# Performance work log

Hardware: AMD Instinct MI355X
Metric: run time of the kernel (lower is better)

Reference implementation:

```python
import jax, jax.numpy as jnp
import numpy as np


def _maxpool(x, k):
    # NCHW max pool with window k, stride k, no padding
    return jax.lax.reduce_window(
        x, -jnp.inf, jax.lax.max,
        window_dimensions=(1, 1, k, k),
        window_strides=(1, 1, k, k),
        padding='VALID')


def setup_inputs() -> dict:
    key = jax.random.key(0)
    k1, k2, k3, k4, k5 = jax.random.split(key, 5)
    return {
        'input_tensor1': jax.random.normal(k1, (8, 128, 56, 56), dtype=jnp.float32),
        'input_tensor2': jax.random.normal(k2, (8, 64, 112, 112), dtype=jnp.float32),
        'input_tensor3': jax.random.normal(k3, (8, 32, 224, 224), dtype=jnp.float32),
        'input_tensor4': jax.random.normal(k4, (8, 16, 448, 448), dtype=jnp.float32),
        'pure_ff': jax.random.normal(k5, (8, 256, 28, 28), dtype=jnp.float32),
    }


def reference(input_tensor1, input_tensor2, input_tensor3, input_tensor4, pure_ff):
    # Original: cat input k times along channels, then maxpool. Pooling is
    # channel-independent, so pool-once-then-tile is mathematically identical
    # (the cat pattern [x,x,...,x] is an exact channel tiling).
    x1 = jnp.tile(_maxpool(input_tensor1, 2), (1, 2, 1, 1))
    x2 = jnp.tile(_maxpool(input_tensor2, 4), (1, 4, 1, 1))
    x3 = jnp.tile(_maxpool(input_tensor3, 8), (1, 8, 1, 1))
    x4 = jnp.tile(_maxpool(input_tensor4, 16), (1, 16, 1, 1))
    return jax.nn.relu(x1 + x2 + x3 + x4 + pure_ff)
```

## Files before the change

kernel.cpp:

```cpp
#include <hip/hip_runtime.h>

#define DEVINL __device__ __forceinline__

DEVINL float fmax4(float4 v) { return fmaxf(fmaxf(v.x, v.y), fmaxf(v.z, v.w)); }
DEVINL float4 max44(float4 a, float4 b) {
    float4 r; r.x = fmaxf(a.x, b.x); r.y = fmaxf(a.y, b.y);
    r.z = fmaxf(a.z, b.z); r.w = fmaxf(a.w, b.w); return r;
}

#define MEMBAR() asm volatile("" ::: "memory")

#define P4O 0
#define P3O 448
#define P2O 1344
#define P1O 3136
#define SCRO 6720
#define LDS_FLOATS 13888

#define LD7(DST, PTR)                                                      \
    { _Pragma("unroll") for (int k = 0; k < 7; ++k)                        \
          DST[k] = *(const float4*)((PTR) + k * 256); }

#define LD7T2(DST, EOFF)                                                   \
    { _Pragma("unroll") for (int k = 0; k < 7; ++k) {                      \
          const int f = k * 64 + lane;                                     \
          DST[k] = *(const float4*)(base2 + (EOFF) + (f / 112) * 12544     \
                                    + (f % 112) * 4); } }

#define LD7T1(DST)                                                         \
    { _Pragma("unroll") for (int k = 0; k < 7; ++k) {                      \
          const int f = k * 64 + lane;                                     \
          DST[k] = *(const float4*)(base1 + (f / 28) * 3136                \
                                    + (f % 28) * 4); } }

#define ACCSET(V) { _Pragma("unroll") for (int k = 0; k < 7; ++k) acc[k] = V[k]; }
#define ACCMAX(V) { _Pragma("unroll") for (int k = 0; k < 7; ++k) acc[k] = max44(acc[k], V[k]); }

#define GATH4(E)                                                           \
    { _Pragma("unroll") for (int k = 0; k < 7; ++k)                        \
          sm[k * 64 + lane] = fmax4(acc[k]);                               \
      MEMBAR();                                                            \
      if (lane < 28) {                                                     \
          float4 ga = *(const float4*)&sm[0 * 112 + 4 * lane];             \
          float4 gb = *(const float4*)&sm[1 * 112 + 4 * lane];             \
          float4 gc = *(const float4*)&sm[2 * 112 + 4 * lane];             \
          float4 gd = *(const float4*)&sm[3 * 112 + 4 * lane];             \
          lds[P4O + (2 * ww + (E)) * 28 + lane] =                          \
              fmax4(max44(max44(ga, gb), max44(gc, gd))); } }

#define T3W(V, H)                                                          \
    { float* smh = sm + (H) * 448;                                         \
      _Pragma("unroll") for (int k = 0; k < 7; ++k)                        \
          smh[k * 64 + lane] = fmax4(V[k]); }
#define T3G(I, H)                                                          \
    { float* smh = sm + (H) * 448;                                         \
      if (lane < 28) {                                                     \
          float2 p0 = *(const float2*)&smh[2 * lane];                      \
          float m = fmaxf(p0.x, p0.y);                                     \
          _Pragma("unroll") for (int r = 1; r < 8; ++r) {                  \
              float2 pr = *(const float2*)&smh[r * 56 + 2 * lane];         \
              m = fmaxf(m, fmaxf(pr.x, pr.y)); }                          \
          lds[P3O + (4 * ww + (I)) * 28 + lane] = m; } }

#define T2W(V, H)                                                          \
    { float* smh = sm + (H) * 448;                                         \
      _Pragma("unroll") for (int k = 0; k < 7; ++k)                        \
          smh[k * 64 + lane] = fmax4(V[k]); }
#define T2G(E, H)                                                          \
    { float* smh = sm + (H) * 448;                                         \
      if (lane < 56) {                                                     \
          _Pragma("unroll") for (int h2 = 0; h2 < 2; ++h2) {               \
              const int o = lane + 56 * h2;                                \
              const int cc = o / 28, j = o % 28;                           \
              float m = fmaxf(fmaxf(smh[cc * 112 + 0 * 28 + j],            \
                                    smh[cc * 112 + 1 * 28 + j]),           \
                              fmaxf(smh[cc * 112 + 2 * 28 + j],            \
                                    smh[cc * 112 + 3 * 28 + j]));          \
              lds[P2O + (8 * ww + 4 * (E) + cc) * 28 + j] = m; } } }

#define T1W(V)                                                             \
    { _Pragma("unroll") for (int k = 0; k < 7; ++k) {                      \
          const int f = k * 64 + lane;                                     \
          float2 hh; hh.x = fmaxf(V[k].x, V[k].y);                         \
          hh.y = fmaxf(V[k].z, V[k].w);                                    \
          *(float2*)&sm[2 * f] = hh; } }
#define T1G()                                                              \
    { _Pragma("unroll") for (int h2 = 0; h2 < 7; ++h2) {                   \
          const int idx = h2 * 64 + lane;                                  \
          const int cc = idx / 28, j = idx % 28;                           \
          lds[P1O + (16 * ww + cc) * 28 + j] =                             \
              fmaxf(sm[cc * 56 + j], sm[cc * 56 + 28 + j]); } }

__global__ __launch_bounds__(512, 2) void fused_all(
    const float* __restrict__ t1, const float* __restrict__ t2,
    const float* __restrict__ t3, const float* __restrict__ t4,
    const float* __restrict__ ff, float* __restrict__ out)
{
    __shared__ __align__(16) float lds[LDS_FLOATS];
    const int tid  = threadIdx.x;
    const int lane = tid & 63;
    const int ww   = tid >> 6;
    const int ph   = blockIdx.x;
    const int b    = blockIdx.y;
    float* sm = &lds[SCRO + ww * 896];

    const float4* FF = (const float4*)ff;
    float4 ffr[4];
    #pragma unroll
    for (int m = 0; m < 3; ++m) {
        const int i4 = tid + 512 * m;
        ffr[m] = FF[(size_t)(b * 256 + i4 / 7) * 196 + ph * 7 + i4 % 7];
    }
    if (tid < 256) {
        const int i4 = tid + 1536;
        ffr[3] = FF[(size_t)(b * 256 + i4 / 7) * 196 + ph * 7 + i4 % 7];
    }

    const float* a4 = t4 + (size_t)b * 3211264 + (2 * ww) * 200704
                    + ph * 16 * 448 + 4 * lane;
    const float* b4 = a4 + 200704;
    const float* c3 = t3 + (size_t)b * 1605632 + (4 * ww) * 50176
                    + ph * 8 * 224 + 4 * lane;
    const float* base2 = t2 + (size_t)b * 802816 + (8 * ww) * 12544
                       + ph * 448;
    const float* base1 = t1 + (size_t)b * 401408 + (16 * ww) * 3136
                       + ph * 112;

    float4 A[7], B[7], acc[7];
    LD7(A, a4);
    LD7(B, a4 + 1792);
    MEMBAR();
    ACCSET(A);
    LD7(A, a4 + 3584); MEMBAR();
    ACCMAX(B);
    LD7(B, a4 + 5376); MEMBAR();
    ACCMAX(A);
    LD7(A, b4); MEMBAR();
    ACCMAX(B);
    LD7(B, b4 + 1792); MEMBAR();
    GATH4(0);
    ACCSET(A);
    LD7(A, b4 + 3584); MEMBAR();
    ACCMAX(B);
    LD7(B, b4 + 5376); MEMBAR();
    ACCMAX(A);
    LD7(A, c3); MEMBAR();
    ACCMAX(B);
    LD7(B, c3 + 50176); MEMBAR();
    GATH4(1);
    T3W(A, 0); LD7(A, c3 + 2 * 50176); MEMBAR(); T3G(0, 0);
    T3W(B, 1); LD7(B, c3 + 3 * 50176); MEMBAR(); T3G(1, 1);
    T3W(A, 0); LD7T2(A, 0);            MEMBAR(); T3G(2, 0);
    T3W(B, 1); LD7T2(B, 50176);        MEMBAR(); T3G(3, 1);
    T2W(A, 0); LD7T1(A);               MEMBAR(); T2G(0, 0);
    T2W(B, 1);                         MEMBAR(); T2G(1, 1);
    T1W(A); MEMBAR(); T1G();

    __syncthreads();

    float4* O = (float4*)out;
    #pragma unroll
    for (int m = 0; m < 4; ++m) {
        if (m < 3 || tid < 256) {
            const int i4 = tid + 512 * m;
            const int ch = i4 / 7, j4 = i4 % 7;
            const float4 x1 = *(const float4*)&lds[P1O + (ch & 127) * 28 + 4 * j4];
            const float4 x2 = *(const float4*)&lds[P2O + (ch & 63)  * 28 + 4 * j4];
            const float4 x3 = *(const float4*)&lds[P3O + (ch & 31)  * 28 + 4 * j4];
            const float4 x4 = *(const float4*)&lds[P4O + (ch & 15)  * 28 + 4 * j4];
            const float4 f  = ffr[m];
            float4 o;
            o.x = fmaxf(x1.x + x2.x + x3.x + x4.x + f.x, 0.0f);
            o.y = fmaxf(x1.y + x2.y + x3.y + x4.y + f.y, 0.0f);
            o.z = fmaxf(x1.z + x2.z + x3.z + x4.z + f.z, 0.0f);
            o.w = fmaxf(x1.w + x2.w + x3.w + x4.w + f.w, 0.0f);
            O[(size_t)(b * 256 + ch) * 196 + ph * 7 + j4] = o;
        }
    }
}

extern "C" void kernel_launch(void* const* d_in, const int* in_sizes, int n_in,
                              void* d_out, int out_size, void* d_ws, size_t ws_size,
                              hipStream_t stream) {
    const float* t1 = (const float*)d_in[0];
    const float* t2 = (const float*)d_in[1];
    const float* t3 = (const float*)d_in[2];
    const float* t4 = (const float*)d_in[3];
    const float* ff = (const float*)d_in[4];
    dim3 grid(28, 8);
    fused_all<<<grid, 512, 0, stream>>>(t1, t2, t3, t4, ff, (float*)d_out);
}
```

Before: 225.2 us.

## Use inline-asm global loads with explicit vmcnt waits and triple buffering

Replaces compiler-generated global loads with inline-asm global_load_dwordx4 and manual s_waitcnt vmcnt counters. A third register buffer lets up to three batches of loads stay in flight while the max reductions run. The ff prefetch is made unconditional with clamped indices so the vmcnt accounting stays fixed. This raises register pressure, and correctness now depends on the hand-counted waits, since the compiler no longer tracks these loads.

```diff
diff --git a/kernel.cpp b/kernel.cpp
--- a/kernel.cpp
+++ b/kernel.cpp
@@ -2,13 +2,22 @@
 
 #define DEVINL __device__ __forceinline__
 
-DEVINL float fmax4(float4 v) { return fmaxf(fmaxf(v.x, v.y), fmaxf(v.z, v.w)); }
-DEVINL float4 max44(float4 a, float4 b) {
-    float4 r; r.x = fmaxf(a.x, b.x); r.y = fmaxf(a.y, b.y);
+typedef float f4 __attribute__((ext_vector_type(4)));
+
+DEVINL float fmax4(f4 v) { return fmaxf(fmaxf(v.x, v.y), fmaxf(v.z, v.w)); }
+DEVINL f4 max44(f4 a, f4 b) {
+    f4 r; r.x = fmaxf(a.x, b.x); r.y = fmaxf(a.y, b.y);
     r.z = fmaxf(a.z, b.z); r.w = fmaxf(a.w, b.w); return r;
 }
 
-#define MEMBAR() asm volatile("" ::: "memory")
+DEVINL f4 ald(const float* p) {
+    f4 r;
+    asm volatile("global_load_dwordx4 %0, %1, off" : "=v"(r) : "v"(p));
+    return r;
+}
+#define VMW(N)                                                             \
+    asm volatile("s_waitcnt vmcnt(" #N ")" ::: "memory");                  \
+    __builtin_amdgcn_sched_barrier(0);
 
 #define P4O 0
 #define P3O 448
@@ -17,21 +26,19 @@
 #define SCRO 6720
 #define LDS_FLOATS 13888
 
-#define LD7(DST, PTR)                                                      \
+#define LD7G(DST, PTR)                                                     \
     { _Pragma("unroll") for (int k = 0; k < 7; ++k)                        \
-          DST[k] = *(const float4*)((PTR) + k * 256); }
+          DST[k] = ald((PTR) + k * 256); }
 
 #define LD7T2(DST, EOFF)                                                   \
     { _Pragma("unroll") for (int k = 0; k < 7; ++k) {                      \
           const int f = k * 64 + lane;                                     \
-          DST[k] = *(const float4*)(base2 + (EOFF) + (f / 112) * 12544     \
-                                    + (f % 112) * 4); } }
+          DST[k] = ald(base2 + (EOFF) + (f / 112) * 12544 + (f % 112) * 4); } }
 
 #define LD7T1(DST)                                                         \
     { _Pragma("unroll") for (int k = 0; k < 7; ++k) {                      \
           const int f = k * 64 + lane;                                     \
-          DST[k] = *(const float4*)(base1 + (f / 28) * 3136                \
-                                    + (f % 28) * 4); } }
+          DST[k] = ald(base1 + (f / 28) * 3136 + (f % 28) * 4); } }
 
 #define ACCSET(V) { _Pragma("unroll") for (int k = 0; k < 7; ++k) acc[k] = V[k]; }
 #define ACCMAX(V) { _Pragma("unroll") for (int k = 0; k < 7; ++k) acc[k] = max44(acc[k], V[k]); }
@@ -39,12 +46,11 @@
 #define GATH4(E)                                                           \
     { _Pragma("unroll") for (int k = 0; k < 7; ++k)                        \
           sm[k * 64 + lane] = fmax4(acc[k]);                               \
-      MEMBAR();                                                            \
       if (lane < 28) {                                                     \
-          float4 ga = *(const float4*)&sm[0 * 112 + 4 * lane];             \
-          float4 gb = *(const float4*)&sm[1 * 112 + 4 * lane];             \
-          float4 gc = *(const float4*)&sm[2 * 112 + 4 * lane];             \
-          float4 gd = *(const float4*)&sm[3 * 112 + 4 * lane];             \
+          f4 ga = *(const f4*)&sm[0 * 112 + 4 * lane];                     \
+          f4 gb = *(const f4*)&sm[1 * 112 + 4 * lane];                     \
+          f4 gc = *(const f4*)&sm[2 * 112 + 4 * lane];                     \
+          f4 gd = *(const f4*)&sm[3 * 112 + 4 * lane];                     \
           lds[P4O + (2 * ww + (E)) * 28 + lane] =                          \
               fmax4(max44(max44(ga, gb), max44(gc, gd))); } }
 
@@ -104,16 +110,13 @@
     const int b    = blockIdx.y;
     float* sm = &lds[SCRO + ww * 896];
 
-    const float4* FF = (const float4*)ff;
-    float4 ffr[4];
+    const float* FF = (const float*)ff;
+    f4 ffr[4];
     #pragma unroll
-    for (int m = 0; m < 3; ++m) {
-        const int i4 = tid + 512 * m;
-        ffr[m] = FF[(size_t)(b * 256 + i4 / 7) * 196 + ph * 7 + i4 % 7];
-    }
-    if (tid < 256) {
-        const int i4 = tid + 1536;
-        ffr[3] = FF[(size_t)(b * 256 + i4 / 7) * 196 + ph * 7 + i4 % 7];
+    for (int m = 0; m < 4; ++m) {
+        const int i4r = tid + 512 * m;
+        const int i4 = i4r < 1792 ? i4r : 1791;
+        ffr[m] = ald(FF + ((size_t)(b * 256 + i4 / 7) * 196 + ph * 7 + i4 % 7) * 4);
     }
 
     const float* a4 = t4 + (size_t)b * 3211264 + (2 * ww) * 200704
@@ -126,50 +129,61 @@
     const float* base1 = t1 + (size_t)b * 401408 + (16 * ww) * 3136
                        + ph * 112;
 
-    float4 A[7], B[7], acc[7];
-    LD7(A, a4);
-    LD7(B, a4 + 1792);
-    MEMBAR();
-    ACCSET(A);
-    LD7(A, a4 + 3584); MEMBAR();
-    ACCMAX(B);
-    LD7(B, a4 + 5376); MEMBAR();
-    ACCMAX(A);
-    LD7(A, b4); MEMBAR();
-    ACCMAX(B);
-    LD7(B, b4 + 1792); MEMBAR();
+    f4 A[7], B[7], C[7], acc[7];
+    LD7G(A, a4);
+    LD7G(B, a4 + 1792);
+    LD7G(C, a4 + 3584);
+    VMW(14) ACCSET(A);
+    LD7G(A, a4 + 5376);
+    VMW(14) ACCMAX(B);
+    LD7G(B, b4);
+    VMW(14) ACCMAX(C);
+    LD7G(C, b4 + 1792);
+    VMW(14) ACCMAX(A);
+    LD7G(A, b4 + 3584);
     GATH4(0);
-    ACCSET(A);
-    LD7(A, b4 + 3584); MEMBAR();
-    ACCMAX(B);
-    LD7(B, b4 + 5376); MEMBAR();
-    ACCMAX(A);
-    LD7(A, c3); MEMBAR();
-    ACCMAX(B);
-    LD7(B, c3 + 50176); MEMBAR();
+    VMW(14) ACCSET(B);
+    LD7G(B, b4 + 5376);
+    VMW(14) ACCMAX(C);
+    LD7G(C, c3);
+    VMW(14) ACCMAX(A);
+    LD7G(A, c3 + 50176);
+    VMW(14) ACCMAX(B);
+    LD7G(B, c3 + 2 * 50176);
     GATH4(1);
-    T3W(A, 0); LD7(A, c3 + 2 * 50176); MEMBAR(); T3G(0, 0);
-    T3W(B, 1); LD7(B, c3 + 3 * 50176); MEMBAR(); T3G(1, 1);
-    T3W(A, 0); LD7T2(A, 0);            MEMBAR(); T3G(2, 0);
-    T3W(B, 1); LD7T2(B, 50176);        MEMBAR(); T3G(3, 1);
-    T2W(A, 0); LD7T1(A);               MEMBAR(); T2G(0, 0);
-    T2W(B, 1);                         MEMBAR(); T2G(1, 1);
-    T1W(A); MEMBAR(); T1G();
+    VMW(14) T3W(C, 0);
+    LD7G(C, c3 + 3 * 50176);
+    T3G(0, 0);
+    VMW(14) T3W(A, 1);
+    LD7T2(A, 0);
+    T3G(1, 1);
+    VMW(14) T3W(B, 0);
+    LD7T2(B, 50176);
+    T3G(2, 0);
+    VMW(14) T3W(C, 1);
+    LD7T1(C);
+    T3G(3, 1);
+    VMW(14) T2W(A, 0);
+    T2G(0, 0);
+    VMW(7)  T2W(B, 1);
+    T2G(1, 1);
+    VMW(0)  T1W(C);
+    T1G();
 
     __syncthreads();
 
-    float4* O = (float4*)out;
+    f4* O = (f4*)out;
     #pragma unroll
     for (int m = 0; m < 4; ++m) {
         if (m < 3 || tid < 256) {
             const int i4 = tid + 512 * m;
             const int ch = i4 / 7, j4 = i4 % 7;
-            const float4 x1 = *(const float4*)&lds[P1O + (ch & 127) * 28 + 4 * j4];
-            const float4 x2 = *(const float4*)&lds[P2O + (ch & 63)  * 28 + 4 * j4];
-            const float4 x3 = *(const float4*)&lds[P3O + (ch & 31)  * 28 + 4 * j4];
-            const float4 x4 = *(const float4*)&lds[P4O + (ch & 15)  * 28 + 4 * j4];
-            const float4 f  = ffr[m];
-            float4 o;
+            const f4 x1 = *(const f4*)&lds[P1O + (ch & 127) * 28 + 4 * j4];
+            const f4 x2 = *(const f4*)&lds[P2O + (ch & 63)  * 28 + 4 * j4];
+            const f4 x3 = *(const f4*)&lds[P3O + (ch & 31)  * 28 + 4 * j4];
+            const f4 x4 = *(const f4*)&lds[P4O + (ch & 15)  * 28 + 4 * j4];
+            const f4 f  = ffr[m];
+            f4 o;
             o.x = fmaxf(x1.x + x2.x + x3.x + x4.x + f.x, 0.0f);
             o.y = fmaxf(x1.y + x2.y + x3.y + x4.y + f.y, 0.0f);
             o.z = fmaxf(x1.z + x2.z + x3.z + x4.z + f.z, 0.0f);
```

New measurement: 223.1 us. No clear change (-0.9%).
